# Performance work log

Measured on AMD Instinct MI355X. Metric: run time of the kernel, lower is better.

## Reference

```python
import jax, jax.numpy as jnp
import numpy as np

C, N, E = 16, 10000, 40000
OP_DIM, LAY_DIM = 4, 4
NODE_FEAT, CFG_FEAT = 140, 18
GRAPH_IN, GRAPH_OUT, HID = 256, 256, 256
HIDDEN_CH = [256, 256, 256]
N_CONVS = len(HIDDEN_CH) + 1  # 4


def setup_inputs() -> dict:
    key = jax.random.key(0)
    ks = iter(jax.random.split(key, 32))
    inp = {}
    inp['x_node_cfg'] = jax.random.randint(next(ks), (C, N, CFG_FEAT), 0, 8)
    inp['x_feat'] = jax.random.normal(next(ks), (N, NODE_FEAT), dtype=jnp.float32)
    inp['x_op'] = jax.random.randint(next(ks), (N,), 0, 120)
    inp['edge_index'] = jax.random.randint(next(ks), (2, E), 0, N)
    s = 0.05
    inp['emb_op'] = jax.random.normal(next(ks), (120, OP_DIM), dtype=jnp.float32)
    inp['emb_layout'] = jax.random.normal(next(ks), (8, LAY_DIM), dtype=jnp.float32)
    in_dim = OP_DIM + NODE_FEAT + CFG_FEAT * LAY_DIM  # 216
    inp['lin_w'] = jax.random.normal(next(ks), (in_dim, GRAPH_IN), dtype=jnp.float32) * s
    inp['lin_b'] = jnp.zeros((GRAPH_IN,), dtype=jnp.float32)
    # all conv dims are 256 -> stack
    inp['conv_wl'] = jax.random.normal(next(ks), (N_CONVS, GRAPH_IN, GRAPH_IN), dtype=jnp.float32) * s
    inp['conv_bl'] = jnp.zeros((N_CONVS, GRAPH_IN), dtype=jnp.float32)
    inp['conv_wr'] = jax.random.normal(next(ks), (N_CONVS, GRAPH_IN, GRAPH_IN), dtype=jnp.float32) * s
    inp['w1'] = jax.random.normal(next(ks), (GRAPH_OUT, HID), dtype=jnp.float32) * s
    inp['b1'] = jnp.zeros((HID,), dtype=jnp.float32)
    inp['w2'] = jax.random.normal(next(ks), (HID, HID), dtype=jnp.float32) * s
    inp['b2'] = jnp.zeros((HID,), dtype=jnp.float32)
    inp['w3'] = jax.random.normal(next(ks), (HID, 1), dtype=jnp.float32) * s
    inp['b3'] = jnp.zeros((1,), dtype=jnp.float32)
    return inp


def reference(x_node_cfg, x_feat, x_op, edge_index, emb_op, emb_layout,
              lin_w, lin_b, conv_wl, conv_bl, conv_wr, w1, b1, w2, b2, w3, b3):
    c, n = x_node_cfg.shape[0], x_node_cfg.shape[1]
    # feature build: layout-config embedding [C,N,18*4], repeated node feat, op embedding
    cfg = emb_layout[x_node_cfg].reshape(c, n, -1)                    # [C,N,72]
    feat = jnp.broadcast_to(x_feat[None], (c, n, x_feat.shape[1]))    # [C,N,140]
    op = jnp.broadcast_to(emb_op[x_op][None], (c, n, emb_op.shape[1]))# [C,N,4]
    x = jnp.concatenate([feat, cfg, op], axis=2)                      # [C,N,216]
    x = x @ lin_w + lin_b                                             # [C,N,256]

    src, dst = edge_index[0], edge_index[1]
    deg = jnp.zeros((n,), x.dtype).at[dst].add(1.0)
    inv_deg = 1.0 / jnp.maximum(deg, 1.0)                             # scatter-mean denom
    for i in range(conv_wl.shape[0]):
        # SAGEConv: out = lin_l(mean_{j in N(i)} x_j) + lin_r(x_i)
        agg = jnp.zeros_like(x).at[:, dst, :].add(x[:, src, :])
        agg = agg * inv_deg[None, :, None]
        x = jax.nn.relu(agg @ conv_wl[i] + conv_bl[i] + x @ conv_wr[i])

    g = x.mean(axis=1)                                                # [C,256] mean pool
    h = jax.nn.relu(g @ w1 + b1)
    h = jax.nn.relu(h @ w2 + b2)
    out = h @ w3 + b3                                                 # [C,1]
    return out.reshape(-1)
```

## Files before the change

kernel.cpp:

```cpp
#include <hip/hip_runtime.h>

#define N_NODES 10000
#define N_CFG   16
#define N_EDGES 40000
#define UW      512

typedef __attribute__((ext_vector_type(8))) short bf16x8;
typedef __attribute__((ext_vector_type(4))) float floatx4;

__device__ __forceinline__ unsigned short f2bf(float f) {
    union { float f; unsigned int u; } v; v.f = f;
    unsigned int r = (v.u + 0x7fffu + ((v.u >> 16) & 1u)) >> 16;
    return (unsigned short)r;
}
__device__ __forceinline__ float bf2f(unsigned short h) {
    union { unsigned int u; float f; } v; v.u = ((unsigned int)h) << 16;
    return v.f;
}
__device__ __forceinline__ void add8(float* acc, uint4 v) {
    acc[0] += bf2f(v.x & 0xffff); acc[1] += bf2f(v.x >> 16);
    acc[2] += bf2f(v.y & 0xffff); acc[3] += bf2f(v.y >> 16);
    acc[4] += bf2f(v.z & 0xffff); acc[5] += bf2f(v.z >> 16);
    acc[6] += bf2f(v.w & 0xffff); acc[7] += bf2f(v.w >> 16);
}

__device__ __forceinline__ void gl_lds16(const unsigned short* g, unsigned short* l) {
    __builtin_amdgcn_global_load_lds(
        (const __attribute__((address_space(1))) unsigned int*)g,
        (__attribute__((address_space(3))) unsigned int*)l, 16, 0, 0);
}


__global__ __launch_bounds__(256) void k_table(const float* __restrict__ emb_layout,
                                               const float* __restrict__ lin_w,
                                               unsigned short* __restrict__ T) {
    int b = blockIdx.x;
    int j = b >> 3, v = b & 7;
    int d = threadIdx.x;
    float s = 0.f;
#pragma unroll
    for (int t = 0; t < 4; ++t)
        s = fmaf(emb_layout[v * 4 + t], lin_w[(140 + 4 * j + t) * 256 + d], s);
    T[b * 256 + d] = f2bf(s);
}

__global__ __launch_bounds__(256) void k_base(const float* __restrict__ x_feat,
                                              const int* __restrict__ x_op,
                                              const float* __restrict__ emb_op,
                                              const float* __restrict__ lin_w,
                                              const float* __restrict__ lin_b,
                                              unsigned short* __restrict__ base) {
    __shared__ float xf[20][144];
    const int tid = threadIdx.x;
    const int n0 = blockIdx.x * 20;
    for (int j = tid; j < 20 * 140; j += 256)
        xf[j / 140][j % 140] = x_feat[(n0 + j / 140) * 140 + (j % 140)];
    if (tid < 80) {
        int i = tid >> 2, t = tid & 3;
        xf[i][140 + t] = emb_op[x_op[n0 + i] * 4 + t];
    }
    __syncthreads();
    const int d = tid;
    float acc[20];
#pragma unroll
    for (int i = 0; i < 20; ++i) acc[i] = 0.f;
    for (int k = 0; k < 140; ++k) {
        float w = lin_w[k * 256 + d];
#pragma unroll
        for (int i = 0; i < 20; ++i) acc[i] = fmaf(xf[i][k], w, acc[i]);
    }
#pragma unroll
    for (int t = 0; t < 4; ++t) {
        float w = lin_w[(212 + t) * 256 + d];
#pragma unroll
        for (int i = 0; i < 20; ++i) acc[i] = fmaf(xf[i][140 + t], w, acc[i]);
    }
    float bb = lin_b[d];
#pragma unroll
    for (int i = 0; i < 20; ++i)
        base[(n0 + i) * 256 + d] = f2bf(acc[i] + bb);
}

template <int CH>
__global__ __launch_bounds__(256) void k_x0(const unsigned short* __restrict__ base,
                                            const unsigned short* __restrict__ T,
                                            const int* __restrict__ cfg,
                                            unsigned short* __restrict__ U,
                                            int cc) {
    __shared__ int idx[8][18];
    const int tid = threadIdx.x;
    const int n0 = blockIdx.x * 8;
    const int cy = blockIdx.y;
    const int cg = cc * CH + cy;
    if (tid < 144) {
        int nl = tid / 18, j = tid % 18;
        idx[nl][j] = cfg[((size_t)cg * N_NODES + n0 + nl) * 18 + j];
    }
    __syncthreads();
    const int nl = tid >> 5;
    const int colg = (tid & 31) * 8;
    const int n = n0 + nl;
    float acc[8];
    uint4 bv = *(const uint4*)(base + n * 256 + colg);
    acc[0] = bf2f(bv.x & 0xffff); acc[1] = bf2f(bv.x >> 16);
    acc[2] = bf2f(bv.y & 0xffff); acc[3] = bf2f(bv.y >> 16);
    acc[4] = bf2f(bv.z & 0xffff); acc[5] = bf2f(bv.z >> 16);
    acc[6] = bf2f(bv.w & 0xffff); acc[7] = bf2f(bv.w >> 16);
#pragma unroll
    for (int j = 0; j < 18; ++j) {
        uint4 tv = *(const uint4*)(T + (j * 8 + idx[nl][j]) * 256 + colg);
        add8(acc, tv);
    }
    uint4 o;
    o.x = (unsigned int)f2bf(acc[0]) | ((unsigned int)f2bf(acc[1]) << 16);
    o.y = (unsigned int)f2bf(acc[2]) | ((unsigned int)f2bf(acc[3]) << 16);
    o.z = (unsigned int)f2bf(acc[4]) | ((unsigned int)f2bf(acc[5]) << 16);
    o.w = (unsigned int)f2bf(acc[6]) | ((unsigned int)f2bf(acc[7]) << 16);
    *(uint4*)(U + ((size_t)cy * N_NODES + n) * UW + 256 + colg) = o;
}


__global__ void k_deg(const int* __restrict__ ei, int* __restrict__ deg) {
    int e = blockIdx.x * 256 + threadIdx.x;
    if (e < N_EDGES) atomicAdd(&deg[ei[N_EDGES + e]], 1);
}

__global__ __launch_bounds__(256) void k_scan(const int* __restrict__ deg,
                                              int* __restrict__ coff) {
    __shared__ int part[257];
    int t = threadIdx.x;
    const int CHk = 40;
    int start = t * CHk;
    int s = 0;
    for (int i = 0; i < CHk; ++i) {
        int idx = start + i;
        if (idx < N_NODES) s += deg[idx];
    }
    part[t + 1] = s;
    if (t == 0) part[0] = 0;
    __syncthreads();
    if (t == 0)
        for (int i = 1; i <= 256; ++i) part[i] += part[i - 1];
    __syncthreads();
    int run = part[t];
    for (int i = 0; i < CHk; ++i) {
        int idx = start + i;
        if (idx < N_NODES) { coff[idx] = run; run += deg[idx]; }
    }
    if (t == 0) coff[N_NODES] = part[256];
}

__global__ void k_invdeg(const int* __restrict__ deg, float* __restrict__ invd) {
    int n = blockIdx.x * 256 + threadIdx.x;
    if (n < N_NODES) invd[n] = 1.0f / fmaxf((float)deg[n], 1.0f);
}

__global__ void k_fill(const int* __restrict__ ei, const int* __restrict__ coff,
                       int* __restrict__ cur, int* __restrict__ csrc) {
    int e = blockIdx.x * 256 + threadIdx.x;
    if (e < N_EDGES) {
        int d = ei[N_EDGES + e];
        int s = ei[e];
        int pos = atomicAdd(&cur[d], 1);
        csrc[coff[d] + pos] = s;
    }
}

__global__ void k_wsplit(const float* __restrict__ wl, const float* __restrict__ wr,
                         unsigned short* __restrict__ WT) {
    int t = blockIdx.x * 256 + threadIdx.x;
    int i = t >> 17;
    int r = (t >> 8) & 511;
    int nn = t & 255;
    float w = (r < 256) ? wl[i * 65536 + r * 256 + nn]
                        : wr[i * 65536 + (r - 256) * 256 + nn];
    unsigned short hi = f2bf(w);
    unsigned short lo = f2bf(w - bf2f(hi));
    size_t b = (size_t)i * 262144 + (size_t)nn * 1024;
    WT[b + r] = hi;
    WT[b + 512 + r] = lo;
}


__global__ __launch_bounds__(256) void k_agg(unsigned short* __restrict__ U,
                                             const int* __restrict__ coff,
                                             const int* __restrict__ csrc,
                                             const float* __restrict__ invd) {
    int wave = threadIdx.x >> 6, lane = threadIdx.x & 63;
    int n = blockIdx.x * 4 + wave;
    const size_t cbase = (size_t)blockIdx.y * 4 * N_NODES;
    int e0 = coff[n], e1 = coff[n + 1];
    float acc[4][4];
#pragma unroll
    for (int cy = 0; cy < 4; ++cy)
#pragma unroll
        for (int j = 0; j < 4; ++j) acc[cy][j] = 0.f;
    for (int e = e0; e < e1; ++e) {
        int s = csrc[e];
        const unsigned short* p = U + (cbase + s) * UW + 256 + lane * 4;
#pragma unroll
        for (int cy = 0; cy < 4; ++cy) {
            uint2 v = *(const uint2*)(p + (size_t)cy * N_NODES * UW);
            acc[cy][0] += bf2f(v.x & 0xffff);
            acc[cy][1] += bf2f(v.x >> 16);
            acc[cy][2] += bf2f(v.y & 0xffff);
            acc[cy][3] += bf2f(v.y >> 16);
        }
    }
    float iv = invd[n];
#pragma unroll
    for (int cy = 0; cy < 4; ++cy) {
        uint2 o;
        o.x = (unsigned int)f2bf(acc[cy][0] * iv) |
              ((unsigned int)f2bf(acc[cy][1] * iv) << 16);
        o.y = (unsigned int)f2bf(acc[cy][2] * iv) |
              ((unsigned int)f2bf(acc[cy][3] * iv) << 16);
        *(uint2*)(U + (cbase + (size_t)cy * N_NODES + n) * UW + lane * 4) = o;
    }
}


__global__ __launch_bounds__(256) void k_gemm(unsigned short* __restrict__ U,
                                              const unsigned short* __restrict__ WTl,
                                              const float* __restrict__ bias) {
    __shared__ unsigned short Asm[64 * 32];
    __shared__ unsigned short Bh[256 * 32];
    __shared__ unsigned short Bl[256 * 32];
    const int tid = threadIdx.x;
    const int lane = tid & 63;
    const int wave = tid >> 6;
    const size_t r0 = (size_t)blockIdx.x * 64;

    const int srow = tid >> 2;
    const int gc = (tid & 3) ^ ((srow >> 1) & 3);

    const int colg = lane & 15, kg = lane >> 4, quad = lane >> 4;
    int aoff[4], boff[4];
#pragma unroll
    for (int t = 0; t < 4; ++t) {
        int ar = t * 16 + colg;
        aoff[t] = ar * 32 + ((kg ^ ((ar >> 1) & 3)) << 3);
        int br = wave * 64 + t * 16 + colg;
        boff[t] = br * 32 + ((kg ^ ((br >> 1) & 3)) << 3);
    }

    floatx4 acc[4][4];
#pragma unroll
    for (int i = 0; i < 4; ++i)
#pragma unroll
        for (int j = 0; j < 4; ++j) acc[i][j] = (floatx4){0.f, 0.f, 0.f, 0.f};

    const unsigned short* Arow = U + (r0 + srow) * UW + gc * 8;
    const unsigned short* Wrow = WTl + (size_t)srow * 1024 + gc * 8;

    for (int kt = 0; kt < 512; kt += 32) {
        gl_lds16(Arow + kt, Asm + tid * 8);
#pragma unroll
        for (int q = 0; q < 4; ++q) {
            gl_lds16(Wrow + (size_t)q * 65536 + kt,       Bh + q * 2048 + tid * 8);
            gl_lds16(Wrow + (size_t)q * 65536 + 512 + kt, Bl + q * 2048 + tid * 8);
        }
        __syncthreads();

        bf16x8 a[4], bh[4], bl[4];
#pragma unroll
        for (int t = 0; t < 4; ++t) a[t] = *(const bf16x8*)(Asm + aoff[t]);
#pragma unroll
        for (int t = 0; t < 4; ++t) {
            bh[t] = *(const bf16x8*)(Bh + boff[t]);
            bl[t] = *(const bf16x8*)(Bl + boff[t]);
        }
#pragma unroll
        for (int ti = 0; ti < 4; ++ti)
#pragma unroll
            for (int tj = 0; tj < 4; ++tj)
                acc[ti][tj] = __builtin_amdgcn_mfma_f32_16x16x32_bf16(
                    a[ti], bh[tj], acc[ti][tj], 0, 0, 0);
#pragma unroll
        for (int ti = 0; ti < 4; ++ti)
#pragma unroll
            for (int tj = 0; tj < 4; ++tj)
                acc[ti][tj] = __builtin_amdgcn_mfma_f32_16x16x32_bf16(
                    a[ti], bl[tj], acc[ti][tj], 0, 0, 0);
        __syncthreads();
    }

#pragma unroll
    for (int tj = 0; tj < 4; ++tj) {
        int nn = wave * 64 + tj * 16 + colg;
        float bv = bias[nn];
#pragma unroll
        for (int ti = 0; ti < 4; ++ti) {
#pragma unroll
            for (int r = 0; r < 4; ++r) {
                size_t mm = r0 + (size_t)(ti * 16 + quad * 4 + r);
                float y = acc[ti][tj][r] + bv;
                U[mm * UW + 256 + nn] = f2bf(fmaxf(y, 0.f));
            }
        }
    }
}


template <int CH>
__global__ __launch_bounds__(256) void k_pool(const unsigned short* __restrict__ U,
                                              float* __restrict__ g, int cc) {
    int cy = blockIdx.y;
    int d = threadIdx.x;
    size_t row0 = (size_t)cy * N_NODES + blockIdx.x * 250;
    float s = 0.f;
    for (int i = 0; i < 250; ++i)
        s += bf2f(U[(row0 + i) * UW + 256 + d]);
    atomicAdd(&g[(cc * CH + cy) * 256 + d], s);
}

__global__ __launch_bounds__(256) void k_head(const float* __restrict__ g,
                                              const float* __restrict__ w1,
                                              const float* __restrict__ b1,
                                              const float* __restrict__ w2,
                                              const float* __restrict__ b2,
                                              const float* __restrict__ w3,
                                              const float* __restrict__ b3,
                                              float* __restrict__ out) {
    __shared__ float ha[256];
    __shared__ float hb[256];
    __shared__ float red[4];
    int c = blockIdx.x;
    int d = threadIdx.x;
    ha[d] = g[c * 256 + d] / 10000.0f;
    __syncthreads();
    float s = b1[d];
#pragma unroll 4
    for (int k = 0; k < 256; ++k)
        s = fmaf(ha[k], w1[k * 256 + d], s);
    hb[d] = fmaxf(s, 0.f);
    __syncthreads();
    s = b2[d];
#pragma unroll 4
    for (int k = 0; k < 256; ++k)
        s = fmaf(hb[k], w2[k * 256 + d], s);
    ha[d] = fmaxf(s, 0.f);
    __syncthreads();
    float p = ha[d] * w3[d];
#pragma unroll
    for (int off = 32; off > 0; off >>= 1)
        p += __shfl_down(p, off, 64);
    if ((d & 63) == 0) red[d >> 6] = p;
    __syncthreads();
    if (d == 0)
        out[c] = red[0] + red[1] + red[2] + red[3] + b3[0];
}

__global__ void k_wsfail(float* __restrict__ out, float v) {
    out[threadIdx.x] = v;
}


extern "C" void kernel_launch(void* const* d_in, const int* in_sizes, int n_in,
                              void* d_out, int out_size, void* d_ws, size_t ws_size,
                              hipStream_t stream) {
    const int*   x_node_cfg = (const int*)  d_in[0];
    const float* x_feat     = (const float*)d_in[1];
    const int*   x_op       = (const int*)  d_in[2];
    const int*   edge_index = (const int*)  d_in[3];
    const float* emb_op     = (const float*)d_in[4];
    const float* emb_layout = (const float*)d_in[5];
    const float* lin_w      = (const float*)d_in[6];
    const float* lin_b      = (const float*)d_in[7];
    const float* conv_wl    = (const float*)d_in[8];
    const float* conv_bl    = (const float*)d_in[9];
    const float* conv_wr    = (const float*)d_in[10];
    const float* w1         = (const float*)d_in[11];
    const float* b1         = (const float*)d_in[12];
    const float* w2         = (const float*)d_in[13];
    const float* b2         = (const float*)d_in[14];
    const float* w3         = (const float*)d_in[15];
    const float* b3         = (const float*)d_in[16];
    float* out = (float*)d_out;

    const size_t NEED8  = (size_t)8  * N_NODES * UW * 2 + 7627268;
    const size_t NEED16 = (size_t)16 * N_NODES * UW * 2 + 7627268;
    const int CH = (ws_size >= NEED16) ? 16 : 8;

    unsigned short* U    = (unsigned short*)d_ws;
    unsigned short* base = U + (size_t)CH * N_NODES * UW;
    unsigned short* T    = base + 2560000;
    unsigned short* WT   = T + 36864;
    float* invd = (float*)(WT + 1048576);
    float* g    = invd + 10000;
    int* deg  = (int*)(g + 4096);
    int* coff = deg + 10000;
    int* cur  = coff + 10001;
    int* csrc = cur + 10000;

    if (ws_size < NEED8) {
        k_wsfail<<<1, 16, 0, stream>>>(out, (float)ws_size * 1e-9f);
        return;
    }

    hipMemsetAsync(deg, 0, N_NODES * sizeof(int), stream);
    hipMemsetAsync(cur, 0, N_NODES * sizeof(int), stream);
    hipMemsetAsync(g, 0, 4096 * sizeof(float), stream);

    k_table<<<144, 256, 0, stream>>>(emb_layout, lin_w, T);
    k_base<<<500, 256, 0, stream>>>(x_feat, x_op, emb_op, lin_w, lin_b, base);
    k_deg<<<(N_EDGES + 255) / 256, 256, 0, stream>>>(edge_index, deg);
    k_scan<<<1, 256, 0, stream>>>(deg, coff);
    k_invdeg<<<(N_NODES + 255) / 256, 256, 0, stream>>>(deg, invd);
    k_fill<<<(N_EDGES + 255) / 256, 256, 0, stream>>>(edge_index, coff, cur, csrc);
    k_wsplit<<<2048, 256, 0, stream>>>(conv_wl, conv_wr, WT);

    if (CH == 16) {
        k_x0<16><<<dim3(1250, 16), 256, 0, stream>>>(base, T, x_node_cfg, U, 0);
        for (int i = 0; i < 4; ++i) {
            k_agg<<<dim3(2500, 4), 256, 0, stream>>>(U, coff, csrc, invd);
            k_gemm<<<16 * N_NODES / 64, 256, 0, stream>>>(U, WT + i * 262144,
                                                          conv_bl + i * 256);
        }
        k_pool<16><<<dim3(40, 16), 256, 0, stream>>>(U, g, 0);
    } else {
        for (int cc = 0; cc < 2; ++cc) {
            k_x0<8><<<dim3(1250, 8), 256, 0, stream>>>(base, T, x_node_cfg, U, cc);
            for (int i = 0; i < 4; ++i) {
                k_agg<<<dim3(2500, 2), 256, 0, stream>>>(U, coff, csrc, invd);
                k_gemm<<<8 * N_NODES / 64, 256, 0, stream>>>(U, WT + i * 262144,
                                                             conv_bl + i * 256);
            }
            k_pool<8><<<dim3(40, 8), 256, 0, stream>>>(U, g, cc);
        }
    }

    k_head<<<16, 256, 0, stream>>>(g, w1, b1, w2, b2, w3, b3, out);
}
```

Baseline: 964.9 us.

## Enlarge GEMM tile to 128 rows, widen agg loads, fuse invdeg into scan

The GEMM block now covers 128 rows with 8 waves arranged as 2x4, so each loaded weight tile (hi and lo bf16 split) is reused across twice as many rows. This halves the weight traffic per output row. The aggregation kernel now uses 16-byte loads with each half-wave taking alternate edges, then combines the halves with a cross-lane shuffle. The inverse-degree computation is folded into the scan kernel, removing one launch. The trade-offs are fewer GEMM blocks (1250 in the 16-config path), which means less parallelism per launch, and extra shuffle work in agg.

```diff
diff --git a/kernel.cpp b/kernel.cpp
--- a/kernel.cpp
+++ b/kernel.cpp
@@ -126,7 +126,8 @@
 }
 
 __global__ __launch_bounds__(256) void k_scan(const int* __restrict__ deg,
-                                              int* __restrict__ coff) {
+                                              int* __restrict__ coff,
+                                              float* __restrict__ invd) {
     __shared__ int part[257];
     int t = threadIdx.x;
     const int CHk = 40;
@@ -145,14 +146,13 @@
     int run = part[t];
     for (int i = 0; i < CHk; ++i) {
         int idx = start + i;
-        if (idx < N_NODES) { coff[idx] = run; run += deg[idx]; }
+        if (idx < N_NODES) {
+            int d = deg[idx];
+            coff[idx] = run; run += d;
+            invd[idx] = 1.0f / fmaxf((float)d, 1.0f);
+        }
     }
     if (t == 0) coff[N_NODES] = part[256];
-}
-
-__global__ void k_invdeg(const int* __restrict__ deg, float* __restrict__ invd) {
-    int n = blockIdx.x * 256 + threadIdx.x;
-    if (n < N_NODES) invd[n] = 1.0f / fmaxf((float)deg[n], 1.0f);
 }
 
 __global__ void k_fill(const int* __restrict__ ei, const int* __restrict__ coff,
@@ -186,50 +186,62 @@
                                              const int* __restrict__ coff,
                                              const int* __restrict__ csrc,
                                              const float* __restrict__ invd) {
-    int wave = threadIdx.x >> 6, lane = threadIdx.x & 63;
-    int n = blockIdx.x * 4 + wave;
+    const int wave = threadIdx.x >> 6, lane = threadIdx.x & 63;
+    const int n = blockIdx.x * 4 + wave;
     const size_t cbase = (size_t)blockIdx.y * 4 * N_NODES;
-    int e0 = coff[n], e1 = coff[n + 1];
-    float acc[4][4];
+    const int e0 = coff[n], e1 = coff[n + 1];
+    const int h = lane >> 5;
+    const int cg = (lane & 31) * 8;
+    float acc[4][8];
 #pragma unroll
     for (int cy = 0; cy < 4; ++cy)
 #pragma unroll
-        for (int j = 0; j < 4; ++j) acc[cy][j] = 0.f;
-    for (int e = e0; e < e1; ++e) {
+        for (int j = 0; j < 8; ++j) acc[cy][j] = 0.f;
+    for (int e = e0 + h; e < e1; e += 2) {
         int s = csrc[e];
-        const unsigned short* p = U + (cbase + s) * UW + 256 + lane * 4;
+        const unsigned short* p = U + (cbase + s) * UW + 256 + cg;
 #pragma unroll
         for (int cy = 0; cy < 4; ++cy) {
-            uint2 v = *(const uint2*)(p + (size_t)cy * N_NODES * UW);
-            acc[cy][0] += bf2f(v.x & 0xffff);
-            acc[cy][1] += bf2f(v.x >> 16);
-            acc[cy][2] += bf2f(v.y & 0xffff);
-            acc[cy][3] += bf2f(v.y >> 16);
-        }
-    }
-    float iv = invd[n];
-#pragma unroll
-    for (int cy = 0; cy < 4; ++cy) {
-        uint2 o;
-        o.x = (unsigned int)f2bf(acc[cy][0] * iv) |
-              ((unsigned int)f2bf(acc[cy][1] * iv) << 16);
-        o.y = (unsigned int)f2bf(acc[cy][2] * iv) |
-              ((unsigned int)f2bf(acc[cy][3] * iv) << 16);
-        *(uint2*)(U + (cbase + (size_t)cy * N_NODES + n) * UW + lane * 4) = o;
-    }
-}
-
-
-__global__ __launch_bounds__(256) void k_gemm(unsigned short* __restrict__ U,
+            uint4 v = *(const uint4*)(p + (size_t)cy * N_NODES * UW);
+            add8(acc[cy], v);
+        }
+    }
+#pragma unroll
+    for (int cy = 0; cy < 4; ++cy)
+#pragma unroll
+        for (int j = 0; j < 8; ++j)
+            acc[cy][j] += __shfl_xor(acc[cy][j], 32, 64);
+    if (h == 0) {
+        float iv = invd[n];
+#pragma unroll
+        for (int cy = 0; cy < 4; ++cy) {
+            uint4 o;
+            o.x = (unsigned int)f2bf(acc[cy][0] * iv) |
+                  ((unsigned int)f2bf(acc[cy][1] * iv) << 16);
+            o.y = (unsigned int)f2bf(acc[cy][2] * iv) |
+                  ((unsigned int)f2bf(acc[cy][3] * iv) << 16);
+            o.z = (unsigned int)f2bf(acc[cy][4] * iv) |
+                  ((unsigned int)f2bf(acc[cy][5] * iv) << 16);
+            o.w = (unsigned int)f2bf(acc[cy][6] * iv) |
+                  ((unsigned int)f2bf(acc[cy][7] * iv) << 16);
+            *(uint4*)(U + (cbase + (size_t)cy * N_NODES + n) * UW + cg) = o;
+        }
+    }
+}
+
+
+__global__ __launch_bounds__(512) void k_gemm(unsigned short* __restrict__ U,
                                               const unsigned short* __restrict__ WTl,
                                               const float* __restrict__ bias) {
-    __shared__ unsigned short Asm[64 * 32];
+    __shared__ unsigned short Asm[128 * 32];
     __shared__ unsigned short Bh[256 * 32];
     __shared__ unsigned short Bl[256 * 32];
     const int tid = threadIdx.x;
     const int lane = tid & 63;
     const int wave = tid >> 6;
-    const size_t r0 = (size_t)blockIdx.x * 64;
+    const int wm = wave >> 2;
+    const int wn = wave & 3;
+    const size_t r0 = (size_t)blockIdx.x * 128;
 
     const int srow = tid >> 2;
     const int gc = (tid & 3) ^ ((srow >> 1) & 3);
@@ -238,9 +250,9 @@
     int aoff[4], boff[4];
 #pragma unroll
     for (int t = 0; t < 4; ++t) {
-        int ar = t * 16 + colg;
+        int ar = wm * 64 + t * 16 + colg;
         aoff[t] = ar * 32 + ((kg ^ ((ar >> 1) & 3)) << 3);
-        int br = wave * 64 + t * 16 + colg;
+        int br = wn * 64 + t * 16 + colg;
         boff[t] = br * 32 + ((kg ^ ((br >> 1) & 3)) << 3);
     }
 
@@ -250,16 +262,16 @@
 #pragma unroll
         for (int j = 0; j < 4; ++j) acc[i][j] = (floatx4){0.f, 0.f, 0.f, 0.f};
 
-    const unsigned short* Arow = U + (r0 + srow) * UW + gc * 8;
-    const unsigned short* Wrow = WTl + (size_t)srow * 1024 + gc * 8;
+    const unsigned short* Arow  = U + (r0 + srow) * UW + gc * 8;
+    const unsigned short* Wrow0 = WTl + (size_t)srow * 1024 + gc * 8;
+    const unsigned short* Wrow1 = WTl + (size_t)(128 + srow) * 1024 + gc * 8;
 
     for (int kt = 0; kt < 512; kt += 32) {
         gl_lds16(Arow + kt, Asm + tid * 8);
-#pragma unroll
-        for (int q = 0; q < 4; ++q) {
-            gl_lds16(Wrow + (size_t)q * 65536 + kt,       Bh + q * 2048 + tid * 8);
-            gl_lds16(Wrow + (size_t)q * 65536 + 512 + kt, Bl + q * 2048 + tid * 8);
-        }
+        gl_lds16(Wrow0 + kt,       Bh + tid * 8);
+        gl_lds16(Wrow1 + kt,       Bh + 4096 + tid * 8);
+        gl_lds16(Wrow0 + 512 + kt, Bl + tid * 8);
+        gl_lds16(Wrow1 + 512 + kt, Bl + 4096 + tid * 8);
         __syncthreads();
 
         bf16x8 a[4], bh[4], bl[4];
@@ -287,13 +299,13 @@
 
 #pragma unroll
     for (int tj = 0; tj < 4; ++tj) {
-        int nn = wave * 64 + tj * 16 + colg;
+        int nn = wn * 64 + tj * 16 + colg;
         float bv = bias[nn];
 #pragma unroll
         for (int ti = 0; ti < 4; ++ti) {
 #pragma unroll
             for (int r = 0; r < 4; ++r) {
-                size_t mm = r0 + (size_t)(ti * 16 + quad * 4 + r);
+                size_t mm = r0 + (size_t)(wm * 64 + ti * 16 + quad * 4 + r);
                 float y = acc[ti][tj][r] + bv;
                 U[mm * UW + 256 + nn] = f2bf(fmaxf(y, 0.f));
             }
@@ -405,8 +417,7 @@
     k_table<<<144, 256, 0, stream>>>(emb_layout, lin_w, T);
     k_base<<<500, 256, 0, stream>>>(x_feat, x_op, emb_op, lin_w, lin_b, base);
     k_deg<<<(N_EDGES + 255) / 256, 256, 0, stream>>>(edge_index, deg);
-    k_scan<<<1, 256, 0, stream>>>(deg, coff);
-    k_invdeg<<<(N_NODES + 255) / 256, 256, 0, stream>>>(deg, invd);
+    k_scan<<<1, 256, 0, stream>>>(deg, coff, invd);
     k_fill<<<(N_EDGES + 255) / 256, 256, 0, stream>>>(edge_index, coff, cur, csrc);
     k_wsplit<<<2048, 256, 0, stream>>>(conv_wl, conv_wr, WT);
 
@@ -414,8 +425,8 @@
         k_x0<16><<<dim3(1250, 16), 256, 0, stream>>>(base, T, x_node_cfg, U, 0);
         for (int i = 0; i < 4; ++i) {
             k_agg<<<dim3(2500, 4), 256, 0, stream>>>(U, coff, csrc, invd);
-            k_gemm<<<16 * N_NODES / 64, 256, 0, stream>>>(U, WT + i * 262144,
-                                                          conv_bl + i * 256);
+            k_gemm<<<16 * N_NODES / 128, 512, 0, stream>>>(U, WT + i * 262144,
+                                                           conv_bl + i * 256);
         }
         k_pool<16><<<dim3(40, 16), 256, 0, stream>>>(U, g, 0);
     } else {
@@ -423,8 +434,8 @@
             k_x0<8><<<dim3(1250, 8), 256, 0, stream>>>(base, T, x_node_cfg, U, cc);
             for (int i = 0; i < 4; ++i) {
                 k_agg<<<dim3(2500, 2), 256, 0, stream>>>(U, coff, csrc, invd);
-                k_gemm<<<8 * N_NODES / 64, 256, 0, stream>>>(U, WT + i * 262144,
-                                                             conv_bl + i * 256);
+                k_gemm<<<8 * N_NODES / 128, 512, 0, stream>>>(U, WT + i * 262144,
+                                                              conv_bl + i * 256);
             }
             k_pool<8><<<dim3(40, 8), 256, 0, stream>>>(U, g, cc);
         }
```

New measurement: 860.1 us. 1.12x faster.
